# Performance work log

Hardware: AMD Instinct MI355X
Metric: run time of the kernel (lower is better)

The kernel has to match this reference:

```python
import jax, jax.numpy as jnp
import numpy as np

EMBED_DIM = 768
NUM_HEADS = 12
HEAD_DIM = EMBED_DIM // NUM_HEADS
BSZ = 8
N_NODE = 512


def setup_inputs() -> dict:
    key = jax.random.key(0)
    ks = jax.random.split(key, 12)
    s = 0.02
    E = EMBED_DIM
    return {
        "query": jax.random.normal(ks[0], (N_NODE, BSZ, E), jnp.float32),
        "attention_bias": jax.random.normal(ks[1], (BSZ, NUM_HEADS, N_NODE, N_NODE), jnp.float32),
        "node_position": jax.random.normal(ks[2], (BSZ, N_NODE, 3), jnp.float32),
        "Wq": jax.random.normal(ks[3], (E, E), jnp.float32) * s,
        "bq": jnp.zeros((E,), jnp.float32),
        "Wk": jax.random.normal(ks[4], (E, E), jnp.float32) * s,
        "bk": jnp.zeros((E,), jnp.float32),
        "Wv": jax.random.normal(ks[5], (E, E), jnp.float32) * s,
        "bv": jnp.zeros((E,), jnp.float32),
        "W1": jax.random.normal(ks[6], (E, 1), jnp.float32) * s,
        "b1": jnp.zeros((1,), jnp.float32),
        "W2": jax.random.normal(ks[7], (E, 1), jnp.float32) * s,
        "b2": jnp.zeros((1,), jnp.float32),
        "W3": jax.random.normal(ks[8], (E, 1), jnp.float32) * s,
        "b3": jnp.zeros((1,), jnp.float32),
    }


def reference(query, attention_bias, node_position, Wq, bq, Wk, bk, Wv, bv,
              W1, b1, W2, b2, W3, b3):
    bsz, n = node_position.shape[:2]
    H = attention_bias.shape[1]
    E = query.shape[-1]
    hd = E // H
    scaling = hd ** -0.5

    # unit direction vectors between node pairs: delta[b,i,j] = pos[j]-pos[i]
    delta = node_position[:, None, :, :] - node_position[:, :, None, :]  # (b,n,n,3)
    dist = jnp.linalg.norm(delta, axis=-1)                               # (b,n,n)
    delta = delta / (dist[..., None] + 1e-5)

    x = jnp.swapaxes(query, 0, 1)  # (b,n,E)
    q = (x @ Wq + bq).reshape(bsz, n, H, hd).transpose(0, 2, 1, 3) * scaling  # (b,h,n,d)
    k = (x @ Wk + bk).reshape(bsz, n, H, hd).transpose(0, 2, 1, 3)
    v = (x @ Wv + bv).reshape(bsz, n, H, hd).transpose(0, 2, 1, 3)

    attn = jnp.einsum('bhid,bhjd->bhij', q, k)
    probs = jax.nn.softmax(attn + attention_bias, axis=-1)  # (b,h,i,j); dropout = identity (eval)

    # rotational aggregation: out[b,i,c,h,d] = sum_j probs[b,h,i,j]*delta[b,i,j,c]*v[b,h,j,d]
    xo = jnp.einsum('bhij,bijc,bhjd->bichd', probs, delta, v).reshape(bsz, n, 3, E)

    f1 = xo[:, :, 0, :] @ W1 + b1  # (b,n,1)
    f2 = xo[:, :, 1, :] @ W2 + b2
    f3 = xo[:, :, 2, :] @ W3 + b3
    return jnp.concatenate([f1, f2, f3], axis=-1).astype(jnp.float32)  # (b,n,3)
```

## Files before the change

### kernel.cpp

```cpp
#include <hip/hip_runtime.h>
#include <math.h>

#define EDIM 768
#define NH 12
#define HD 64
#define BSZ 8
#define NN 512
#define NCAT 1664

typedef short short8 __attribute__((ext_vector_type(8)));
typedef float f32x4 __attribute__((ext_vector_type(4)));

__device__ __forceinline__ unsigned short f2bf(float x) {
    unsigned int u = __float_as_uint(x);
    u = (u + 0x7FFF + ((u >> 16) & 1)) >> 16;
    return (unsigned short)u;
}
__device__ __forceinline__ float bf2f(unsigned short s) {
    return __uint_as_float(((unsigned int)s) << 16);
}
__device__ __forceinline__ void gl2lds16(const void* g, void* l) {
    __builtin_amdgcn_global_load_lds(
        (const __attribute__((address_space(1))) unsigned int*)g,
        (__attribute__((address_space(3))) unsigned int*)l, 16, 0, 0);
}

#define PB_GEOM_END 512
#define PB_TR_END   1664
#define PB_VW_END   1772
#define PB_CVT_END  3308
#define PB_BC_END   3315
#define PREP_BLOCKS 3350

__global__ __launch_bounds__(256) void k_prep(
        const float* __restrict__ query, const float* __restrict__ pos,
        const float* __restrict__ Wq, const float* __restrict__ bq,
        const float* __restrict__ Wk, const float* __restrict__ bk,
        const float* __restrict__ Wv, const float* __restrict__ bv,
        const float* __restrict__ W1, const float* __restrict__ W2,
        const float* __restrict__ W3,
        unsigned short* __restrict__ WT, float* __restrict__ bcat,
        unsigned short* __restrict__ Xb,
        unsigned short* __restrict__ ud0, unsigned short* __restrict__ ud1,
        unsigned short* __restrict__ ud2) {
    __shared__ float sm[1536];
    const int bid = blockIdx.x;
    const int t = threadIdx.x;

    if (bid < PB_GEOM_END) {
        float* psx = sm; float* psy = sm + NN; float* psz = sm + 2 * NN;
        const int b = bid >> 6, i0 = (bid & 63) * 8;
        for (int idx = t; idx < NN; idx += 256) {
            const float* p = pos + ((size_t)b * NN + idx) * 3;
            psx[idx] = p[0]; psy[idx] = p[1]; psz[idx] = p[2];
        }
        __syncthreads();
        const int i = i0 + (t >> 5);
        const float qx = psx[i], qy = psy[i], qz = psz[i];
        const size_t row = ((size_t)b * NN + i) * NN;
        for (int jt = 0; jt < 4; jt++) {
            int j = ((t & 31) + jt * 32) * 4;
            unsigned short s0[4], s1[4], s2[4];
            #pragma unroll
            for (int u = 0; u < 4; u++) {
                float dx = psx[j + u] - qx, dy = psy[j + u] - qy, dz = psz[j + u] - qz;
                float inv = 1.f / (sqrtf(dx * dx + dy * dy + dz * dz) + 1e-5f);
                s0[u] = f2bf(dx * inv); s1[u] = f2bf(dy * inv); s2[u] = f2bf(dz * inv);
            }
            *(uint2*)&ud0[row + j] = make_uint2(s0[0] | ((unsigned)s0[1] << 16), s0[2] | ((unsigned)s0[3] << 16));
            *(uint2*)&ud1[row + j] = make_uint2(s1[0] | ((unsigned)s1[1] << 16), s1[2] | ((unsigned)s1[3] << 16));
            *(uint2*)&ud2[row + j] = make_uint2(s2[0] | ((unsigned)s2[1] << 16), s2[2] | ((unsigned)s2[3] << 16));
        }
    } else if (bid < PB_TR_END) {
        float (*tile)[33] = (float(*)[33])sm;
        const int tb = bid - PB_GEOM_END;
        const int n0 = (tb % 48) * 32, e0 = (tb / 48) * 32;
        const float* src = (n0 < 768) ? Wq : Wk;
        const int ol0 = (n0 < 768) ? n0 : (n0 - 768);
        const int tx = t & 31, ty = t >> 5;
        #pragma unroll
        for (int s = 0; s < 4; s++)
            tile[ty + s * 8][tx] = src[(size_t)(e0 + ty + s * 8) * EDIM + ol0 + tx];
        __syncthreads();
        #pragma unroll
        for (int s = 0; s < 4; s++)
            WT[(size_t)(n0 + ty + s * 8) * EDIM + e0 + tx] = f2bf(tile[tx][ty + s * 8]);
    } else if (bid < PB_VW_END) {
        int idx = (bid - PB_TR_END) * 256 + t;
        int o2 = idx / 768, e = idx - o2 * 768;
        int h = o2 / 3, c = o2 - (o2 / 3) * 3;
        const float* Wc = (c == 0) ? W1 : (c == 1) ? W2 : W3;
        const float4* wvp = (const float4*)(Wv + (size_t)e * EDIM + h * HD);
        const float4* wcp = (const float4*)(Wc + h * HD);
        float s = 0.f;
        #pragma unroll
        for (int d4 = 0; d4 < 16; d4++) {
            float4 a = wvp[d4], b = wcp[d4];
            s += a.x * b.x + a.y * b.y + a.z * b.z + a.w * b.w;
        }
        WT[(size_t)(1536 + o2) * EDIM + e] = f2bf(s);
    } else if (bid < PB_CVT_END) {
        int idx = (bid - PB_VW_END) * 256 + t;
        int m = idx / 96, e8 = (idx - (idx / 96) * 96) * 8;
        int b = m >> 9, i = m & (NN - 1);
        const float* src = query + ((size_t)i * BSZ + b) * EDIM + e8;
        float4 v0 = *(const float4*)src;
        float4 v1 = *(const float4*)(src + 4);
        unsigned int p0 = f2bf(v0.x) | ((unsigned int)f2bf(v0.y) << 16);
        unsigned int p1 = f2bf(v0.z) | ((unsigned int)f2bf(v0.w) << 16);
        unsigned int p2 = f2bf(v1.x) | ((unsigned int)f2bf(v1.y) << 16);
        unsigned int p3 = f2bf(v1.z) | ((unsigned int)f2bf(v1.w) << 16);
        uint4 pk = {p0, p1, p2, p3};
        *(uint4*)&Xb[(size_t)idx * 8] = pk;
    } else if (bid < PB_BC_END) {
        int o = (bid - PB_CVT_END) * 256 + t;
        if (o < NCAT) {
            float v = 0.f;
            if (o < 768) v = bq[o];
            else if (o < 1536) v = bk[o - 768];
            else if (o < 1572) {
                int o2 = o - 1536;
                int h = o2 / 3, c = o2 - (o2 / 3) * 3;
                const float* Wc = (c == 0) ? W1 : (c == 1) ? W2 : W3;
                float s = 0.f;
                for (int d = 0; d < HD; d++) s += bv[h * HD + d] * Wc[h * HD + d];
                v = s;
            }
            bcat[o] = v;
        }
    } else {
        int tid = (bid - PB_BC_END) * 256 + t;
        if (tid < 8832) {
            uint4 z = {0, 0, 0, 0};
            *(uint4*)&WT[(size_t)1572 * EDIM + (size_t)tid * 8] = z;
        }
    }
}

__global__ __launch_bounds__(256) void k_gemm_qkv(
        const unsigned short* __restrict__ Xb, const unsigned short* __restrict__ WT,
        const float* __restrict__ bcat,
        unsigned short* __restrict__ qb, unsigned short* __restrict__ kb,
        float* __restrict__ vwb) {
    __shared__ short As[8 * 64 * 8];
    __shared__ short Bs[8 * 128 * 8];
    const int t = threadIdx.x;
    const int m0 = blockIdx.x * 64, n0 = blockIdx.y * 128;
    const int w = t >> 6, lane = t & 63, quad = lane >> 4, ln = lane & 15;
    const int wm = (w & 1) * 32, wn = (w >> 1) * 64;

    f32x4 acc[2][4];
    #pragma unroll
    for (int mi = 0; mi < 2; mi++)
        #pragma unroll
        for (int ni = 0; ni < 4; ni++) acc[mi][ni] = (f32x4){0.f, 0.f, 0.f, 0.f};

    for (int k0 = 0; k0 < EDIM; k0 += 64) {
        __syncthreads();
        #pragma unroll
        for (int is = 0; is < 2; is++) {
            int slot = is * 256 + t;
            int g = slot >> 6, m = slot & 63;
            gl2lds16(Xb + (size_t)(m0 + m) * EDIM + k0 + g * 8, &As[(size_t)(is * 256 + w * 64) * 8]);
        }
        #pragma unroll
        for (int is = 0; is < 4; is++) {
            int slot = is * 256 + t;
            int g = slot >> 7, n = slot & 127;
            gl2lds16(WT + (size_t)(n0 + n) * EDIM + k0 + g * 8, &Bs[(size_t)(is * 256 + w * 64) * 8]);
        }
        __syncthreads();
        #pragma unroll
        for (int s = 0; s < 2; s++) {
            short8 af[2], bf[4];
            #pragma unroll
            for (int mi = 0; mi < 2; mi++)
                af[mi] = *(const short8*)&As[(size_t)((s * 4 + quad) * 64 + wm + mi * 16 + ln) * 8];
            #pragma unroll
            for (int ni = 0; ni < 4; ni++)
                bf[ni] = *(const short8*)&Bs[(size_t)((s * 4 + quad) * 128 + wn + ni * 16 + ln) * 8];
            #pragma unroll
            for (int mi = 0; mi < 2; mi++)
                #pragma unroll
                for (int ni = 0; ni < 4; ni++)
                    acc[mi][ni] = __builtin_amdgcn_mfma_f32_16x16x32_bf16(af[mi], bf[ni], acc[mi][ni], 0, 0, 0);
        }
    }

    #pragma unroll
    for (int mi = 0; mi < 2; mi++) {
        #pragma unroll
        for (int r = 0; r < 4; r++) {
            int mg = m0 + wm + mi * 16 + quad * 4 + r;
            int b_ = mg >> 9, i_ = mg & (NN - 1);
            #pragma unroll
            for (int ni = 0; ni < 4; ni++) {
                int o = n0 + wn + ni * 16 + ln;
                float val = acc[mi][ni][r] + bcat[o];
                if (o < 768) {
                    int h = o >> 6, d = o & 63;
                    qb[(((size_t)b_ * NH + h) * NN + i_) * HD + d] = f2bf(val * 0.125f);
                } else if (o < 1536) {
                    int o2 = o - 768;
                    int h = o2 >> 6, d = o2 & 63;
                    kb[(((size_t)b_ * NH + h) * NN + i_) * HD + d] = f2bf(val);
                } else if (o < 1572) {
                    int o2 = o - 1536;
                    int h = o2 / 3, c = o2 - (o2 / 3) * 3;
                    vwb[(((size_t)b_ * NH + h) * NN + i_) * 3 + c] = val;
                }
            }
        }
    }
}

__global__ __launch_bounds__(256, 4) void k_attn(
        const unsigned short* __restrict__ qb, const unsigned short* __restrict__ kb,
        const float* __restrict__ vwb, const float* __restrict__ bias,
        const unsigned short* __restrict__ ud0, const unsigned short* __restrict__ ud1,
        const unsigned short* __restrict__ ud2,
        float* __restrict__ mp, float* __restrict__ lp,
        float* __restrict__ a0p, float* __restrict__ a1p, float* __restrict__ a2p) {
    __shared__ short Ks[2 * 8 * 64 * 8];
    __shared__ float ws0[128], ws1[128], ws2[128];

    const int t = threadIdx.x;
    const int bid = blockIdx.x;
    const int h = bid % NH;
    const int r1 = bid / NH;
    const int js = r1 & 3;
    const int it = (r1 >> 2) & 7;
    const int b = r1 >> 5;
    const int i0 = it * 64;
    const int jb = js * 128;
    const int w = t >> 6, lane = t & 63, quad = lane >> 4, ln = lane & 15;
    const size_t bh = (size_t)b * NH + h;

    #pragma unroll
    for (int is = 0; is < 4; is++) {
        int slot = is * 256 + t;
        int tile = slot >> 9, dg = (slot >> 6) & 7, j = slot & 63;
        gl2lds16(kb + (bh * NN + jb + tile * 64 + j) * HD + dg * 8,
                 &Ks[(size_t)(is * 256 + w * 64) * 8]);
    }
    for (int idx = t; idx < 384; idx += 256) {
        float v = vwb[bh * (NN * 3) + (size_t)jb * 3 + idx];
        int jj = idx / 3, c = idx - (idx / 3) * 3;
        if (c == 0) ws0[jj] = v; else if (c == 1) ws1[jj] = v; else ws2[jj] = v;
    }

    const int ig = i0 + w * 16 + ln;
    const unsigned short* qrow = qb + (bh * NN + ig) * HD;
    short8 qf0 = *(const short8*)(qrow + quad * 8);
    short8 qf1 = *(const short8*)(qrow + 32 + quad * 8);
    const float* brow = bias + (bh * NN + ig) * NN + jb;
    const size_t udrow = ((size_t)b * NN + ig) * NN + jb;

    f32x4 acc[8];
    #pragma unroll
    for (int s8 = 0; s8 < 8; s8++) {
        int off = (s8 >> 2) * 64 + (s8 & 3) * 16 + quad * 4;
        acc[s8] = *(const f32x4*)(brow + off);
    }

    __syncthreads();

    #pragma unroll
    for (int s8 = 0; s8 < 8; s8++) {
        int tile = s8 >> 2, sub = s8 & 3;
        short8 af0 = *(const short8*)&Ks[(size_t)((tile * 8 + quad) * 64 + sub * 16 + ln) * 8];
        short8 af1 = *(const short8*)&Ks[(size_t)((tile * 8 + 4 + quad) * 64 + sub * 16 + ln) * 8];
        acc[s8] = __builtin_amdgcn_mfma_f32_16x16x32_bf16(af0, qf0, acc[s8], 0, 0, 0);
        acc[s8] = __builtin_amdgcn_mfma_f32_16x16x32_bf16(af1, qf1, acc[s8], 0, 0, 0);
    }

    float m_r = acc[0][0];
    #pragma unroll
    for (int s8 = 0; s8 < 8; s8++)
        #pragma unroll
        for (int r = 0; r < 4; r++) m_r = fmaxf(m_r, acc[s8][r]);
    m_r = fmaxf(m_r, __shfl_xor(m_r, 16, 64));
    m_r = fmaxf(m_r, __shfl_xor(m_r, 32, 64));

    float l_r = 0.f, a0 = 0.f, a1 = 0.f, a2 = 0.f;
    #pragma unroll
    for (int s8 = 0; s8 < 8; s8++) {
        int off = (s8 >> 2) * 64 + (s8 & 3) * 16 + quad * 4;
        f32x4 w0v = *(const f32x4*)&ws0[off];
        f32x4 w1v = *(const f32x4*)&ws1[off];
        f32x4 w2v = *(const f32x4*)&ws2[off];
        union { uint2 u; unsigned short s[4]; } U0, U1, U2;
        U0.u = *(const uint2*)&ud0[udrow + off];
        U1.u = *(const uint2*)&ud1[udrow + off];
        U2.u = *(const uint2*)&ud2[udrow + off];
        #pragma unroll
        for (int r = 0; r < 4; r++) {
            float p = __expf(acc[s8][r] - m_r);
            l_r += p;
            a0 = fmaf(p * bf2f(U0.s[r]), w0v[r], a0);
            a1 = fmaf(p * bf2f(U1.s[r]), w1v[r], a1);
            a2 = fmaf(p * bf2f(U2.s[r]), w2v[r], a2);
        }
    }

    #pragma unroll
    for (int off = 16; off <= 32; off <<= 1) {
        l_r += __shfl_xor(l_r, off, 64);
        a0  += __shfl_xor(a0, off, 64);
        a1  += __shfl_xor(a1, off, 64);
        a2  += __shfl_xor(a2, off, 64);
    }
    if (quad == 0) {
        size_t o4 = (bh * NN + ig) * 4 + js;
        mp[o4] = m_r; lp[o4] = l_r;
        a0p[o4] = a0; a1p[o4] = a1; a2p[o4] = a2;
    }
}

__global__ __launch_bounds__(256) void k_finalize(
        const float* __restrict__ mp, const float* __restrict__ lp,
        const float* __restrict__ a0p, const float* __restrict__ a1p,
        const float* __restrict__ a2p,
        const float* __restrict__ b1, const float* __restrict__ b2,
        const float* __restrict__ b3, float* __restrict__ out) {
    int idx = blockIdx.x * 256 + threadIdx.x;
    int b = idx >> 9, i = idx & (NN - 1);
    float s0 = 0.f, s1 = 0.f, s2 = 0.f;
    #pragma unroll
    for (int h = 0; h < NH; h++) {
        size_t base = (((size_t)b * NH + h) * NN + i) * 4;
        f32x4 mv = *(const f32x4*)&mp[base];
        f32x4 lv = *(const f32x4*)&lp[base];
        f32x4 A0 = *(const f32x4*)&a0p[base];
        f32x4 A1 = *(const f32x4*)&a1p[base];
        f32x4 A2 = *(const f32x4*)&a2p[base];
        float M = fmaxf(fmaxf(mv[0], mv[1]), fmaxf(mv[2], mv[3]));
        float L = 0.f, c0 = 0.f, c1 = 0.f, c2 = 0.f;
        #pragma unroll
        for (int js = 0; js < 4; js++) {
            float e = __expf(mv[js] - M);
            L = fmaf(e, lv[js], L);
            c0 = fmaf(e, A0[js], c0);
            c1 = fmaf(e, A1[js], c1);
            c2 = fmaf(e, A2[js], c2);
        }
        float inv = 1.f / L;
        s0 = fmaf(c0, inv, s0);
        s1 = fmaf(c1, inv, s1);
        s2 = fmaf(c2, inv, s2);
    }
    float* op = out + (size_t)idx * 3;
    op[0] = s0 + b1[0];
    op[1] = s1 + b2[0];
    op[2] = s2 + b3[0];
}

extern "C" void kernel_launch(void* const* d_in, const int* in_sizes, int n_in,
                              void* d_out, int out_size, void* d_ws, size_t ws_size,
                              hipStream_t stream) {
    const float* query = (const float*)d_in[0];
    const float* bias  = (const float*)d_in[1];
    const float* pos   = (const float*)d_in[2];
    const float* Wq = (const float*)d_in[3];
    const float* bq = (const float*)d_in[4];
    const float* Wk = (const float*)d_in[5];
    const float* bk = (const float*)d_in[6];
    const float* Wv = (const float*)d_in[7];
    const float* bv = (const float*)d_in[8];
    const float* W1 = (const float*)d_in[9];
    const float* b1 = (const float*)d_in[10];
    const float* W2 = (const float*)d_in[11];
    const float* b2 = (const float*)d_in[12];
    const float* W3 = (const float*)d_in[13];
    const float* b3 = (const float*)d_in[14];
    float* out = (float*)d_out;

    char* p = (char*)d_ws;
    unsigned short* WT = (unsigned short*)p; p += (size_t)NCAT * EDIM * 2;
    float* bcat = (float*)p;                 p += (size_t)NCAT * 4;
    unsigned short* Xb = (unsigned short*)p; p += (size_t)BSZ * NN * EDIM * 2;
    unsigned short* qb = (unsigned short*)p; p += (size_t)BSZ * NH * NN * HD * 2;
    unsigned short* kb = (unsigned short*)p; p += (size_t)BSZ * NH * NN * HD * 2;
    float* vwb = (float*)p;                  p += (size_t)BSZ * NH * NN * 3 * 4;
    unsigned short* ud0 = (unsigned short*)p; p += (size_t)BSZ * NN * NN * 2;
    unsigned short* ud1 = (unsigned short*)p; p += (size_t)BSZ * NN * NN * 2;
    unsigned short* ud2 = (unsigned short*)p; p += (size_t)BSZ * NN * NN * 2;
    const size_t PSZ = (size_t)BSZ * NH * NN * 4;
    float* mp  = (float*)p; p += PSZ * 4;
    float* lp  = (float*)p; p += PSZ * 4;
    float* a0p = (float*)p; p += PSZ * 4;
    float* a1p = (float*)p; p += PSZ * 4;
    float* a2p = (float*)p; p += PSZ * 4;

    k_prep<<<PREP_BLOCKS, 256, 0, stream>>>(query, pos, Wq, bq, Wk, bk, Wv, bv,
                                            W1, W2, W3, WT, bcat, Xb, ud0, ud1, ud2);
    dim3 g2(64, 13);
    k_gemm_qkv<<<g2, 256, 0, stream>>>(Xb, WT, bcat, qb, kb, vwb);
    k_attn<<<BSZ * NH * 8 * 4, 256, 0, stream>>>(qb, kb, vwb, bias, ud0, ud1, ud2,
                                                 mp, lp, a0p, a1p, a2p);
    k_finalize<<<BSZ * NN / 256, 256, 0, stream>>>(mp, lp, a0p, a1p, a2p, b1, b2, b3, out);
}
```

Measured before the change: 281.3 us.

## Interleave direction vectors and transpose attention MFMA layout with swizzled LDS Q/K

```diff
diff --git a/kernel.cpp b/kernel.cpp
--- a/kernel.cpp
+++ b/kernel.cpp
@@ -41,8 +41,7 @@
         const float* __restrict__ W3,
         unsigned short* __restrict__ WT, float* __restrict__ bcat,
         unsigned short* __restrict__ Xb,
-        unsigned short* __restrict__ ud0, unsigned short* __restrict__ ud1,
-        unsigned short* __restrict__ ud2) {
+        unsigned int* __restrict__ udp) {
     __shared__ float sm[1536];
     const int bid = blockIdx.x;
     const int t = threadIdx.x;
@@ -60,16 +59,17 @@
         const size_t row = ((size_t)b * NN + i) * NN;
         for (int jt = 0; jt < 4; jt++) {
             int j = ((t & 31) + jt * 32) * 4;
-            unsigned short s0[4], s1[4], s2[4];
+            unsigned int s0[4], s1[4], s2[4];
             #pragma unroll
             for (int u = 0; u < 4; u++) {
                 float dx = psx[j + u] - qx, dy = psy[j + u] - qy, dz = psz[j + u] - qz;
                 float inv = 1.f / (sqrtf(dx * dx + dy * dy + dz * dz) + 1e-5f);
                 s0[u] = f2bf(dx * inv); s1[u] = f2bf(dy * inv); s2[u] = f2bf(dz * inv);
             }
-            *(uint2*)&ud0[row + j] = make_uint2(s0[0] | ((unsigned)s0[1] << 16), s0[2] | ((unsigned)s0[3] << 16));
-            *(uint2*)&ud1[row + j] = make_uint2(s1[0] | ((unsigned)s1[1] << 16), s1[2] | ((unsigned)s1[3] << 16));
-            *(uint2*)&ud2[row + j] = make_uint2(s2[0] | ((unsigned)s2[1] << 16), s2[2] | ((unsigned)s2[3] << 16));
+            uint4 A = {s0[0] | (s1[0] << 16), s2[0], s0[1] | (s1[1] << 16), s2[1]};
+            uint4 B = {s0[2] | (s1[2] << 16), s2[2], s0[3] | (s1[3] << 16), s2[3]};
+            *(uint4*)&udp[(row + j) * 2]     = A;
+            *(uint4*)&udp[(row + j) * 2 + 4] = B;
         }
     } else if (bid < PB_TR_END) {
         float (*tile)[33] = (float(*)[33])sm;
@@ -217,11 +217,11 @@
 __global__ __launch_bounds__(256, 4) void k_attn(
         const unsigned short* __restrict__ qb, const unsigned short* __restrict__ kb,
         const float* __restrict__ vwb, const float* __restrict__ bias,
-        const unsigned short* __restrict__ ud0, const unsigned short* __restrict__ ud1,
-        const unsigned short* __restrict__ ud2,
+        const unsigned int* __restrict__ udp,
         float* __restrict__ mp, float* __restrict__ lp,
         float* __restrict__ a0p, float* __restrict__ a1p, float* __restrict__ a2p) {
-    __shared__ short Ks[2 * 8 * 64 * 8];
+    __shared__ uint4 Qs[64 * 8];
+    __shared__ uint4 Ks[128 * 8];
     __shared__ float ws0[128], ws1[128], ws2[128];
 
     const int t = threadIdx.x;
@@ -236,84 +236,103 @@
     const int w = t >> 6, lane = t & 63, quad = lane >> 4, ln = lane & 15;
     const size_t bh = (size_t)b * NH + h;
 
-    #pragma unroll
-    for (int is = 0; is < 4; is++) {
-        int slot = is * 256 + t;
-        int tile = slot >> 9, dg = (slot >> 6) & 7, j = slot & 63;
-        gl2lds16(kb + (bh * NN + jb + tile * 64 + j) * HD + dg * 8,
-                 &Ks[(size_t)(is * 256 + w * 64) * 8]);
-    }
-    for (int idx = t; idx < 384; idx += 256) {
-        float v = vwb[bh * (NN * 3) + (size_t)jb * 3 + idx];
-        int jj = idx / 3, c = idx - (idx / 3) * 3;
-        if (c == 0) ws0[jj] = v; else if (c == 1) ws1[jj] = v; else ws2[jj] = v;
-    }
-
-    const int ig = i0 + w * 16 + ln;
-    const unsigned short* qrow = qb + (bh * NN + ig) * HD;
-    short8 qf0 = *(const short8*)(qrow + quad * 8);
-    short8 qf1 = *(const short8*)(qrow + 32 + quad * 8);
-    const float* brow = bias + (bh * NN + ig) * NN + jb;
-    const size_t udrow = ((size_t)b * NN + ig) * NN + jb;
-
+    const uint4* qg = (const uint4*)(qb + (bh * NN + i0) * HD);
+    const uint4* kg = (const uint4*)(kb + (bh * NN + jb) * HD);
+    const int rr = t >> 3, cc = t & 7;
+    uint4 qv0 = qg[t];
+    uint4 qv1 = qg[256 + t];
+    uint4 kv0 = kg[t];
+    uint4 kv1 = kg[256 + t];
+    uint4 kv2 = kg[512 + t];
+    uint4 kv3 = kg[768 + t];
+    float wv0 = vwb[bh * (NN * 3) + (size_t)jb * 3 + t];
+    float wv1 = (t < 128) ? vwb[bh * (NN * 3) + (size_t)jb * 3 + 256 + t] : 0.f;
+
+    const float* bbase = bias + (bh * NN + i0 + w * 16 + quad * 4) * NN + jb + ln;
     f32x4 acc[8];
     #pragma unroll
-    for (int s8 = 0; s8 < 8; s8++) {
-        int off = (s8 >> 2) * 64 + (s8 & 3) * 16 + quad * 4;
-        acc[s8] = *(const f32x4*)(brow + off);
-    }
-
+    for (int jsub = 0; jsub < 8; jsub++)
+        #pragma unroll
+        for (int r = 0; r < 4; r++)
+            acc[jsub][r] = bbase[r * NN + jsub * 16];
+
+    const int sw = cc ^ (rr & 7);
+    Qs[rr * 8 + sw] = qv0;
+    Qs[(rr + 32) * 8 + sw] = qv1;
+    Ks[rr * 8 + sw] = kv0;
+    Ks[(rr + 32) * 8 + sw] = kv1;
+    Ks[(rr + 64) * 8 + sw] = kv2;
+    Ks[(rr + 96) * 8 + sw] = kv3;
+    {
+        int jj = t / 3, c = t - (t / 3) * 3;
+        if (c == 0) ws0[jj] = wv0; else if (c == 1) ws1[jj] = wv0; else ws2[jj] = wv0;
+        if (t < 128) {
+            int t2 = 256 + t;
+            int jj2 = t2 / 3, c2 = t2 - (t2 / 3) * 3;
+            if (c2 == 0) ws0[jj2] = wv1; else if (c2 == 1) ws1[jj2] = wv1; else ws2[jj2] = wv1;
+        }
+    }
     __syncthreads();
 
-    #pragma unroll
-    for (int s8 = 0; s8 < 8; s8++) {
-        int tile = s8 >> 2, sub = s8 & 3;
-        short8 af0 = *(const short8*)&Ks[(size_t)((tile * 8 + quad) * 64 + sub * 16 + ln) * 8];
-        short8 af1 = *(const short8*)&Ks[(size_t)((tile * 8 + 4 + quad) * 64 + sub * 16 + ln) * 8];
-        acc[s8] = __builtin_amdgcn_mfma_f32_16x16x32_bf16(af0, qf0, acc[s8], 0, 0, 0);
-        acc[s8] = __builtin_amdgcn_mfma_f32_16x16x32_bf16(af1, qf1, acc[s8], 0, 0, 0);
+    const int qrow = w * 16 + ln;
+    short8 a0f = *(const short8*)&Qs[qrow * 8 + (quad ^ (qrow & 7))];
+    short8 a1f = *(const short8*)&Qs[qrow * 8 + ((quad + 4) ^ (qrow & 7))];
+    #pragma unroll
+    for (int jsub = 0; jsub < 8; jsub++) {
+        int krow = jsub * 16 + ln;
+        short8 b0f = *(const short8*)&Ks[krow * 8 + (quad ^ (krow & 7))];
+        short8 b1f = *(const short8*)&Ks[krow * 8 + ((quad + 4) ^ (krow & 7))];
+        acc[jsub] = __builtin_amdgcn_mfma_f32_16x16x32_bf16(a0f, b0f, acc[jsub], 0, 0, 0);
+        acc[jsub] = __builtin_amdgcn_mfma_f32_16x16x32_bf16(a1f, b1f, acc[jsub], 0, 0, 0);
     }
 
     float m_r = acc[0][0];
     #pragma unroll
-    for (int s8 = 0; s8 < 8; s8++)
-        #pragma unroll
-        for (int r = 0; r < 4; r++) m_r = fmaxf(m_r, acc[s8][r]);
-    m_r = fmaxf(m_r, __shfl_xor(m_r, 16, 64));
-    m_r = fmaxf(m_r, __shfl_xor(m_r, 32, 64));
-
-    float l_r = 0.f, a0 = 0.f, a1 = 0.f, a2 = 0.f;
-    #pragma unroll
-    for (int s8 = 0; s8 < 8; s8++) {
-        int off = (s8 >> 2) * 64 + (s8 & 3) * 16 + quad * 4;
-        f32x4 w0v = *(const f32x4*)&ws0[off];
-        f32x4 w1v = *(const f32x4*)&ws1[off];
-        f32x4 w2v = *(const f32x4*)&ws2[off];
-        union { uint2 u; unsigned short s[4]; } U0, U1, U2;
-        U0.u = *(const uint2*)&ud0[udrow + off];
-        U1.u = *(const uint2*)&ud1[udrow + off];
-        U2.u = *(const uint2*)&ud2[udrow + off];
+    for (int jsub = 0; jsub < 8; jsub++)
+        #pragma unroll
+        for (int r = 0; r < 4; r++) m_r = fmaxf(m_r, acc[jsub][r]);
+    #pragma unroll
+    for (int off = 1; off < 64; off <<= 1) m_r = fmaxf(m_r, __shfl_xor(m_r, off, 64));
+
+    const unsigned int* udbase = udp + (((size_t)b * NN + i0 + w * 16 + quad * 4) * NN + jb + ln) * 2;
+    float lr[4] = {0.f, 0.f, 0.f, 0.f};
+    float A0[4] = {0.f, 0.f, 0.f, 0.f};
+    float A1[4] = {0.f, 0.f, 0.f, 0.f};
+    float A2[4] = {0.f, 0.f, 0.f, 0.f};
+    #pragma unroll
+    for (int jsub = 0; jsub < 8; jsub++) {
+        float w0 = ws0[jsub * 16 + ln];
+        float w1 = ws1[jsub * 16 + ln];
+        float w2 = ws2[jsub * 16 + ln];
         #pragma unroll
         for (int r = 0; r < 4; r++) {
-            float p = __expf(acc[s8][r] - m_r);
-            l_r += p;
-            a0 = fmaf(p * bf2f(U0.s[r]), w0v[r], a0);
-            a1 = fmaf(p * bf2f(U1.s[r]), w1v[r], a1);
-            a2 = fmaf(p * bf2f(U2.s[r]), w2v[r], a2);
-        }
-    }
-
-    #pragma unroll
-    for (int off = 16; off <= 32; off <<= 1) {
-        l_r += __shfl_xor(l_r, off, 64);
-        a0  += __shfl_xor(a0, off, 64);
-        a1  += __shfl_xor(a1, off, 64);
-        a2  += __shfl_xor(a2, off, 64);
-    }
-    if (quad == 0) {
-        size_t o4 = (bh * NN + ig) * 4 + js;
-        mp[o4] = m_r; lp[o4] = l_r;
-        a0p[o4] = a0; a1p[o4] = a1; a2p[o4] = a2;
+            uint2 U = *(const uint2*)&udbase[((size_t)r * NN + jsub * 16) * 2];
+            float p = __expf(acc[jsub][r] - m_r);
+            lr[r] += p;
+            A0[r] = fmaf(p * bf2f((unsigned short)(U.x & 0xFFFF)), w0, A0[r]);
+            A1[r] = fmaf(p * bf2f((unsigned short)(U.x >> 16)), w1, A1[r]);
+            A2[r] = fmaf(p * bf2f((unsigned short)(U.y & 0xFFFF)), w2, A2[r]);
+        }
+    }
+
+    #pragma unroll
+    for (int off = 1; off < 16; off <<= 1) {
+        #pragma unroll
+        for (int r = 0; r < 4; r++) {
+            lr[r] += __shfl_xor(lr[r], off, 64);
+            A0[r] += __shfl_xor(A0[r], off, 64);
+            A1[r] += __shfl_xor(A1[r], off, 64);
+            A2[r] += __shfl_xor(A2[r], off, 64);
+        }
+    }
+    if (ln == 0) {
+        #pragma unroll
+        for (int r = 0; r < 4; r++) {
+            int ig = i0 + w * 16 + quad * 4 + r;
+            size_t o4 = (bh * NN + ig) * 4 + js;
+            mp[o4] = m_r; lp[o4] = lr[r];
+            a0p[o4] = A0[r]; a1p[o4] = A1[r]; a2p[o4] = A2[r];
+        }
     }
 }
 
@@ -382,9 +401,7 @@
     unsigned short* qb = (unsigned short*)p; p += (size_t)BSZ * NH * NN * HD * 2;
     unsigned short* kb = (unsigned short*)p; p += (size_t)BSZ * NH * NN * HD * 2;
     float* vwb = (float*)p;                  p += (size_t)BSZ * NH * NN * 3 * 4;
-    unsigned short* ud0 = (unsigned short*)p; p += (size_t)BSZ * NN * NN * 2;
-    unsigned short* ud1 = (unsigned short*)p; p += (size_t)BSZ * NN * NN * 2;
-    unsigned short* ud2 = (unsigned short*)p; p += (size_t)BSZ * NN * NN * 2;
+    unsigned int* udp = (unsigned int*)p;    p += (size_t)BSZ * NN * NN * 8;
     const size_t PSZ = (size_t)BSZ * NH * NN * 4;
     float* mp  = (float*)p; p += PSZ * 4;
     float* lp  = (float*)p; p += PSZ * 4;
@@ -393,10 +410,10 @@
     float* a2p = (float*)p; p += PSZ * 4;
 
     k_prep<<<PREP_BLOCKS, 256, 0, stream>>>(query, pos, Wq, bq, Wk, bk, Wv, bv,
-                                            W1, W2, W3, WT, bcat, Xb, ud0, ud1, ud2);
+                                            W1, W2, W3, WT, bcat, Xb, udp);
     dim3 g2(64, 13);
     k_gemm_qkv<<<g2, 256, 0, stream>>>(Xb, WT, bcat, qb, kb, vwb);
-    k_attn<<<BSZ * NH * 8 * 4, 256, 0, stream>>>(qb, kb, vwb, bias, ud0, ud1, ud2,
+    k_attn<<<BSZ * NH * 8 * 4, 256, 0, stream>>>(qb, kb, vwb, bias, udp,
                                                  mp, lp, a0p, a1p, a2p);
     k_finalize<<<BSZ * NN / 256, 256, 0, stream>>>(mp, lp, a0p, a1p, a2p, b1, b2, b3, out);
 }
```

Result: faster. 252.1 us (-10.4%).
